# Optimization experiments

Hardware: AMD Instinct MI355X
Metric: run time of the kernel (lower is better)

Reference implementation:

```python
import jax, jax.numpy as jnp
import numpy as np

N = 50000      # nodes
R = 3          # relation types
E = 200000     # edges per relation
DIN, DHID, DOUT = 128, 128, 64


def _hetero_graphconv(x, src, dst, W, b):
    """Sum over relations of dgl GraphConv(norm='both') applied per relation.
    x:[N,d_in], src/dst:[R,E], W:[R,d_in,d_out], b:[R,d_out] -> [N,d_out]"""
    Rr, Ee = src.shape
    n = x.shape[0]
    off = (jnp.arange(Rr) * n)[:, None]            # per-relation segment offset
    src_f = (src + off).reshape(-1)                # [R*E]
    dst_f = (dst + off).reshape(-1)
    ones = jnp.ones((Rr * Ee,), x.dtype)
    out_deg = jax.ops.segment_sum(ones, src_f, num_segments=Rr * n).reshape(Rr, n)
    in_deg = jax.ops.segment_sum(ones, dst_f, num_segments=Rr * n).reshape(Rr, n)
    out_norm = jnp.maximum(out_deg, 1.0) ** -0.5   # dgl clamps deg to min 1
    in_norm = jnp.maximum(in_deg, 1.0) ** -0.5
    # gather src features, scaled by per-relation out-degree norm: [R,E,d_in]
    msgs = x[src] * jnp.take_along_axis(out_norm, src, axis=1)[..., None]
    agg = jax.ops.segment_sum(msgs.reshape(Rr * Ee, -1), dst_f,
                              num_segments=Rr * n).reshape(Rr, n, -1)
    agg = agg * in_norm[..., None]                 # [R,N,d_in]
    # per-relation linear then sum over relations (HeteroGraphConv 'sum')
    return jnp.einsum('rnd,rdo->no', agg, W) + b.sum(axis=0)


def setup_inputs() -> dict:
    key = jax.random.key(0)
    ks = jax.random.split(key, 7)
    x = jax.random.normal(ks[0], (N, DIN), jnp.float32)
    src = jax.random.randint(ks[1], (R, E), 0, N)
    dst = jax.random.randint(ks[2], (R, E), 0, N)
    W1 = jax.random.normal(ks[3], (R, DIN, DHID), jnp.float32) / np.sqrt(DIN).astype(np.float32)
    b1 = jax.random.normal(ks[4], (R, DHID), jnp.float32) * 0.01
    W2 = jax.random.normal(ks[5], (R, DHID, DOUT), jnp.float32) / np.sqrt(DHID).astype(np.float32)
    b2 = jax.random.normal(ks[6], (R, DOUT), jnp.float32) * 0.01
    return {"x": x, "W1": W1, "b1": b1, "W2": W2, "b2": b2, "src": src, "dst": dst}


def reference(x, W1, b1, W2, b2, src, dst):
    h = jax.nn.relu(_hetero_graphconv(x, src, dst, W1, b1))
    return _hetero_graphconv(h, src, dst, W2, b2)
```

## Files before the change

kernel.cpp:

```cpp
#include <hip/hip_runtime.h>

#define N_NODES 50000
#define N_REL   3
#define N_EDGE  200000
#define RN      (N_REL * N_NODES)
#define RE      (N_REL * N_EDGE)

typedef short bf16x8 __attribute__((ext_vector_type(8)));
typedef float f32x4  __attribute__((ext_vector_type(4)));

__global__ __launch_bounds__(256) void deg_count_kernel(
    const int* __restrict__ src, const int* __restrict__ dst,
    float* __restrict__ odeg, float* __restrict__ ideg)
{
    int i = blockIdx.x * 256 + threadIdx.x;
    if (i >= RE) return;
    int r = i / N_EDGE;
    unsafeAtomicAdd(&odeg[r * N_NODES + src[i]], 1.0f);
    unsafeAtomicAdd(&ideg[r * N_NODES + dst[i]], 1.0f);
}

__global__ __launch_bounds__(256) void norm_kernel(
    float* __restrict__ odeg, float* __restrict__ ideg)
{
    int i = blockIdx.x * 256 + threadIdx.x;
    if (i >= RN) return;
    odeg[i] = rsqrtf(fmaxf(odeg[i], 1.0f));
    ideg[i] = rsqrtf(fmaxf(ideg[i], 1.0f));
}

__global__ __launch_bounds__(256) void scan1_kernel(
    const float* __restrict__ ideg, int* __restrict__ off, int* __restrict__ bsums)
{
    __shared__ int tsum[256];
    int tid  = threadIdx.x;
    int base = blockIdx.x * 1024 + tid * 4;
    int c[4], s = 0;
    #pragma unroll
    for (int j = 0; j < 4; ++j) {
        int idx = base + j;
        c[j] = (idx < N_NODES)
             ? (int)(ideg[idx] + ideg[N_NODES + idx] + ideg[2 * N_NODES + idx]) : 0;
        s += c[j];
    }
    tsum[tid] = s;
    __syncthreads();
    #pragma unroll
    for (int d = 1; d < 256; d <<= 1) {
        int v   = tsum[tid];
        int add = (tid >= d) ? tsum[tid - d] : 0;
        __syncthreads();
        tsum[tid] = v + add;
        __syncthreads();
    }
    int run = tsum[tid] - s;
    #pragma unroll
    for (int j = 0; j < 4; ++j) {
        if (base + j < N_NODES) off[base + j] = run;
        run += c[j];
    }
    if (tid == 255) bsums[blockIdx.x] = tsum[255];
}

__global__ __launch_bounds__(256) void scan2_kernel(int* __restrict__ bsums, int nb)
{
    __shared__ int t[256];
    int tid = threadIdx.x;
    int v0  = (tid < nb) ? bsums[tid] : 0;
    t[tid] = v0;
    __syncthreads();
    #pragma unroll
    for (int d = 1; d < 256; d <<= 1) {
        int v   = t[tid];
        int add = (tid >= d) ? t[tid - d] : 0;
        __syncthreads();
        t[tid] = v + add;
        __syncthreads();
    }
    if (tid < nb) bsums[tid] = t[tid] - v0;
}

__global__ __launch_bounds__(256) void scan3_kernel(
    int* __restrict__ off, int* __restrict__ cursor, const int* __restrict__ bsums)
{
    int tid  = threadIdx.x;
    int base = blockIdx.x * 1024 + tid * 4;
    int add  = bsums[blockIdx.x];
    #pragma unroll
    for (int j = 0; j < 4; ++j) {
        if (base + j < N_NODES) {
            int v = off[base + j] + add;
            off[base + j]    = v;
            cursor[base + j] = v;
        }
    }
    if (blockIdx.x == 0 && tid == 0) off[N_NODES] = RE;
}

__global__ __launch_bounds__(256) void fill_kernel(
    const int* __restrict__ src, const int* __restrict__ dst,
    const float* __restrict__ onorm, const float* __restrict__ inorm,
    int* __restrict__ cursor, int2* __restrict__ csr)
{
    int i = blockIdx.x * 256 + threadIdx.x;
    if (i >= N_EDGE) return;
    int r = blockIdx.y;
    int s = src[r * N_EDGE + i];
    int t = dst[r * N_EDGE + i];
    float wv = onorm[r * N_NODES + s] * inorm[r * N_NODES + t];
    int pos = atomicAdd(&cursor[t], 1);
    csr[pos] = make_int2(r * N_NODES + s, __float_as_int(wv));
}

__device__ __forceinline__ unsigned short f2bf(float f) {
    unsigned u = __float_as_uint(f);
    u = (u + 0x7fffu + ((u >> 16) & 1u)) >> 16;
    return (unsigned short)u;
}
__device__ __forceinline__ unsigned pack_bf2(float lo, float hi) {
    return (unsigned)f2bf(lo) | ((unsigned)f2bf(hi) << 16);
}

__global__ __launch_bounds__(256) void wtrans_kernel(
    const float* __restrict__ W, unsigned short* __restrict__ Wtf,
    int ncols, int total)
{
    int i = blockIdx.x * 256 + threadIdx.x;
    if (i >= total) return;
    int rel = i / (128 * ncols);
    int rem = i - rel * 128 * ncols;
    int k   = rem / ncols;
    int n   = rem - k * ncols;
    int f   = (rel * (ncols / 16) + (n >> 4)) * 4 + (k >> 5);
    int idx = f * 512 + ((k & 31) >> 3) * 128 + (n & 15) * 8 + (k & 7);
    Wtf[idx] = f2bf(W[i]);
}

template <bool ABF16, int NCOLS>
__global__ __launch_bounds__(256) void gemm_mfma(
    const void* __restrict__ Av, const unsigned short* __restrict__ Wtf,
    unsigned short* __restrict__ Y, int nrows)
{
    __shared__ unsigned As[64 * 68];
    __shared__ unsigned Ws[2][4096];

    const int tid = threadIdx.x;
    const int mt  = blockIdx.x * 64;
    const uint4* Wt4 = (const uint4*)Wtf;

    if constexpr (ABF16) {
        const uint4* Ab = (const uint4*)Av;
        #pragma unroll
        for (int p = 0; p < 4; ++p) {
            int q   = p * 256 + tid;
            int row = q >> 4, w4 = q & 15;
            int gr  = mt + row;
            uint4 v = make_uint4(0u, 0u, 0u, 0u);
            if (gr < nrows) v = Ab[(size_t)gr * 16 + w4];
            As[row * 68 + w4 * 4 + 0] = v.x;
            As[row * 68 + w4 * 4 + 1] = v.y;
            As[row * 68 + w4 * 4 + 2] = v.z;
            As[row * 68 + w4 * 4 + 3] = v.w;
        }
    } else {
        const float* A = (const float*)Av;
        #pragma unroll
        for (int p = 0; p < 16; ++p) {
            int q   = tid + p * 256;
            int row = q >> 6, wc = q & 63;
            int gr  = mt + row;
            float2 v = make_float2(0.f, 0.f);
            if (gr < nrows) v = *reinterpret_cast<const float2*>(&A[(size_t)gr * 128 + wc * 2]);
            As[row * 68 + wc] = pack_bf2(v.x, v.y);
        }
    }

    #pragma unroll
    for (int p = 0; p < 4; ++p) {
        uint4 v = Wt4[tid + p * 256];
        *reinterpret_cast<uint4*>(&Ws[0][(tid + p * 256) * 4]) = v;
    }
    __syncthreads();

    const int w  = tid >> 6;
    const int l  = tid & 63;
    const int g  = l >> 4;
    const int lr = l & 15;
    const int ar = w * 16 + lr;

    bf16x8 a[4];
    #pragma unroll
    for (int kb = 0; kb < 4; ++kb)
        a[kb] = *reinterpret_cast<const bf16x8*>(&As[ar * 68 + kb * 16 + g * 4]);

    constexpr int TPR  = NCOLS / 16;
    constexpr int NGRP = 3 * NCOLS / 64;
    const int boff = (g * 16 + lr) * 4;

    int cur = 0;
    #pragma unroll 1
    for (int grp = 0; grp < NGRP; ++grp) {
        uint4 st[4];
        if (grp + 1 < NGRP) {
            #pragma unroll
            for (int p = 0; p < 4; ++p)
                st[p] = Wt4[(grp + 1) * 1024 + tid + p * 256];
        }

        f32x4 acc[4];
        #pragma unroll
        for (int ct4 = 0; ct4 < 4; ++ct4) {
            acc[ct4] = (f32x4){0.f, 0.f, 0.f, 0.f};
            #pragma unroll
            for (int kb = 0; kb < 4; ++kb) {
                bf16x8 b = *reinterpret_cast<const bf16x8*>(
                    &Ws[cur][(ct4 * 4 + kb) * 256 + boff]);
                acc[ct4] = __builtin_amdgcn_mfma_f32_16x16x32_bf16(a[kb], b, acc[ct4], 0, 0, 0);
            }
        }

        int gct0 = grp * 4;
        int rel  = gct0 / TPR;
        int cb   = (gct0 % TPR) * 16;
        #pragma unroll
        for (int i = 0; i < 4; ++i) {
            int grow = mt + w * 16 + g * 4 + i;
            if (grow < nrows) {
                size_t rowbase = ((size_t)rel * N_NODES + grow) * NCOLS + cb;
                #pragma unroll
                for (int ct4 = 0; ct4 < 4; ++ct4)
                    Y[rowbase + ct4 * 16 + lr] = f2bf(acc[ct4][i]);
            }
        }

        if (grp + 1 < NGRP) {
            #pragma unroll
            for (int p = 0; p < 4; ++p)
                *reinterpret_cast<uint4*>(&Ws[cur ^ 1][(tid + p * 256) * 4]) = st[p];
        }
        __syncthreads();
        cur ^= 1;
    }
}

__global__ __launch_bounds__(256) void agg128_kernel(
    const unsigned* __restrict__ Y, const int2* __restrict__ csr,
    const int* __restrict__ off, const float* __restrict__ b, unsigned* __restrict__ hbf)
{
    int wid  = (blockIdx.x * 256 + threadIdx.x) >> 6;
    int lane = threadIdx.x & 63;
    if (wid >= N_NODES) return;

    int e = off[wid], end = off[wid + 1];
    float a0 = 0.f, a1 = 0.f;

    for (; e + 8 <= end; e += 8) {
        int2 p[8]; unsigned y[8];
        #pragma unroll
        for (int j = 0; j < 8; ++j) p[j] = csr[e + j];
        #pragma unroll
        for (int j = 0; j < 8; ++j) y[j] = Y[(size_t)p[j].x * 64 + lane];
        #pragma unroll
        for (int j = 0; j < 8; ++j) {
            float wv = __int_as_float(p[j].y);
            a0 = fmaf(wv, __uint_as_float(y[j] << 16), a0);
            a1 = fmaf(wv, __uint_as_float(y[j] & 0xffff0000u), a1);
        }
    }
    if (e + 4 <= end) {
        int2 p[4]; unsigned y[4];
        #pragma unroll
        for (int j = 0; j < 4; ++j) p[j] = csr[e + j];
        #pragma unroll
        for (int j = 0; j < 4; ++j) y[j] = Y[(size_t)p[j].x * 64 + lane];
        #pragma unroll
        for (int j = 0; j < 4; ++j) {
            float wv = __int_as_float(p[j].y);
            a0 = fmaf(wv, __uint_as_float(y[j] << 16), a0);
            a1 = fmaf(wv, __uint_as_float(y[j] & 0xffff0000u), a1);
        }
        e += 4;
    }
    for (; e < end; ++e) {
        int2 p = csr[e];
        float wv = __int_as_float(p.y);
        unsigned y = Y[(size_t)p.x * 64 + lane];
        a0 = fmaf(wv, __uint_as_float(y << 16), a0);
        a1 = fmaf(wv, __uint_as_float(y & 0xffff0000u), a1);
    }

    int d = lane * 2;
    float o0 = a0 + b[d]     + b[128 + d]     + b[256 + d];
    float o1 = a1 + b[d + 1] + b[128 + d + 1] + b[256 + d + 1];
    hbf[(size_t)wid * 64 + lane] = pack_bf2(fmaxf(o0, 0.f), fmaxf(o1, 0.f));
}

__global__ __launch_bounds__(256) void agg64_kernel(
    const unsigned short* __restrict__ Y, const int2* __restrict__ csr,
    const int* __restrict__ off, const float* __restrict__ b, float* __restrict__ out)
{
    int wid  = (blockIdx.x * 256 + threadIdx.x) >> 6;
    int lane = threadIdx.x & 63;
    if (wid >= N_NODES) return;

    int e = off[wid], end = off[wid + 1];
    float a = 0.f;

    for (; e + 8 <= end; e += 8) {
        int2 p[8]; unsigned short y[8];
        #pragma unroll
        for (int j = 0; j < 8; ++j) p[j] = csr[e + j];
        #pragma unroll
        for (int j = 0; j < 8; ++j) y[j] = Y[(size_t)p[j].x * 64 + lane];
        #pragma unroll
        for (int j = 0; j < 8; ++j)
            a = fmaf(__int_as_float(p[j].y),
                     __uint_as_float(((unsigned)y[j]) << 16), a);
    }
    if (e + 4 <= end) {
        int2 p[4]; unsigned short y[4];
        #pragma unroll
        for (int j = 0; j < 4; ++j) p[j] = csr[e + j];
        #pragma unroll
        for (int j = 0; j < 4; ++j) y[j] = Y[(size_t)p[j].x * 64 + lane];
        #pragma unroll
        for (int j = 0; j < 4; ++j)
            a = fmaf(__int_as_float(p[j].y),
                     __uint_as_float(((unsigned)y[j]) << 16), a);
        e += 4;
    }
    for (; e < end; ++e) {
        int2 p = csr[e];
        a = fmaf(__int_as_float(p.y),
                 __uint_as_float(((unsigned)Y[(size_t)p.x * 64 + lane]) << 16), a);
    }

    float bs = b[lane] + b[64 + lane] + b[128 + lane];
    out[(size_t)wid * 64 + lane] = a + bs;
}

extern "C" void kernel_launch(void* const* d_in, const int* in_sizes, int n_in,
                              void* d_out, int out_size, void* d_ws, size_t ws_size,
                              hipStream_t stream)
{
    const float* x   = (const float*)d_in[0];
    const float* W1  = (const float*)d_in[1];
    const float* b1  = (const float*)d_in[2];
    const float* W2  = (const float*)d_in[3];
    const float* b2  = (const float*)d_in[4];
    const int*   src = (const int*)d_in[5];
    const int*   dst = (const int*)d_in[6];
    float*       out = (float*)d_out;

    char* w = (char*)d_ws;
    float* onorm  = (float*)w;                 w += (size_t)RN * 4;
    float* inorm  = (float*)w;                 w += (size_t)RN * 4;
    int*   off    = (int*)w;                   w += (size_t)(N_NODES + 1) * 4;
    int*   cursor = (int*)w;                   w += (size_t)N_NODES * 4;
    int*   bsums  = (int*)w;                   w += 1024;
    w = (char*)(((uintptr_t)w + 255) & ~(uintptr_t)255);
    int2*  csr    = (int2*)w;                  w += (size_t)RE * 8;
    unsigned* hbf = (unsigned*)w;              w += (size_t)N_NODES * 64 * 4;
    unsigned short* Ybf = (unsigned short*)w;  w += (size_t)N_REL * N_NODES * 128 * 2;
    unsigned short* Wt1 = (unsigned short*)w;  w += (size_t)N_REL * 128 * 128 * 2;
    unsigned short* Wt2 = (unsigned short*)w;

    const int SCAN_BLOCKS = (N_NODES + 1023) / 1024;
    const int mtiles = (N_NODES + 63) / 64;

    wtrans_kernel<<<(3 * 128 * 128 + 255) / 256, 256, 0, stream>>>(W1, Wt1, 128, 3 * 128 * 128);
    wtrans_kernel<<<(3 * 128 * 64 + 255) / 256, 256, 0, stream>>>(W2, Wt2, 64, 3 * 128 * 64);

    hipMemsetAsync(onorm, 0, (size_t)2 * RN * 4, stream);
    deg_count_kernel<<<(RE + 255) / 256, 256, 0, stream>>>(src, dst, onorm, inorm);

    scan1_kernel<<<SCAN_BLOCKS, 256, 0, stream>>>(inorm, off, bsums);
    scan2_kernel<<<1, 256, 0, stream>>>(bsums, SCAN_BLOCKS);
    scan3_kernel<<<SCAN_BLOCKS, 256, 0, stream>>>(off, cursor, bsums);

    norm_kernel<<<(RN + 255) / 256, 256, 0, stream>>>(onorm, inorm);
    fill_kernel<<<dim3((N_EDGE + 255) / 256, N_REL), 256, 0, stream>>>(
        src, dst, onorm, inorm, cursor, csr);

    gemm_mfma<false, 128><<<mtiles, 256, 0, stream>>>(x, Wt1, Ybf, N_NODES);
    agg128_kernel<<<(N_NODES + 3) / 4, 256, 0, stream>>>((const unsigned*)Ybf, csr, off, b1, hbf);

    gemm_mfma<true, 64><<<mtiles, 256, 0, stream>>>(hbf, Wt2, Ybf, N_NODES);
    agg64_kernel<<<(N_NODES + 3) / 4, 256, 0, stream>>>(Ybf, csr, off, b2, out);
}
```

Measured before the change: 306.7 us.

## Fuse layer-1 GEMM with degree counting and fold norm into scan

```diff
diff --git a/kernel.cpp b/kernel.cpp
--- a/kernel.cpp
+++ b/kernel.cpp
@@ -5,112 +5,12 @@
 #define N_EDGE  200000
 #define RN      (N_REL * N_NODES)
 #define RE      (N_REL * N_EDGE)
+#define GEMM1_BLKS 782
+#define DEG_BLKS   2344
+#define SCAN_BLOCKS 49
 
 typedef short bf16x8 __attribute__((ext_vector_type(8)));
 typedef float f32x4  __attribute__((ext_vector_type(4)));
-
-__global__ __launch_bounds__(256) void deg_count_kernel(
-    const int* __restrict__ src, const int* __restrict__ dst,
-    float* __restrict__ odeg, float* __restrict__ ideg)
-{
-    int i = blockIdx.x * 256 + threadIdx.x;
-    if (i >= RE) return;
-    int r = i / N_EDGE;
-    unsafeAtomicAdd(&odeg[r * N_NODES + src[i]], 1.0f);
-    unsafeAtomicAdd(&ideg[r * N_NODES + dst[i]], 1.0f);
-}
-
-__global__ __launch_bounds__(256) void norm_kernel(
-    float* __restrict__ odeg, float* __restrict__ ideg)
-{
-    int i = blockIdx.x * 256 + threadIdx.x;
-    if (i >= RN) return;
-    odeg[i] = rsqrtf(fmaxf(odeg[i], 1.0f));
-    ideg[i] = rsqrtf(fmaxf(ideg[i], 1.0f));
-}
-
-__global__ __launch_bounds__(256) void scan1_kernel(
-    const float* __restrict__ ideg, int* __restrict__ off, int* __restrict__ bsums)
-{
-    __shared__ int tsum[256];
-    int tid  = threadIdx.x;
-    int base = blockIdx.x * 1024 + tid * 4;
-    int c[4], s = 0;
-    #pragma unroll
-    for (int j = 0; j < 4; ++j) {
-        int idx = base + j;
-        c[j] = (idx < N_NODES)
-             ? (int)(ideg[idx] + ideg[N_NODES + idx] + ideg[2 * N_NODES + idx]) : 0;
-        s += c[j];
-    }
-    tsum[tid] = s;
-    __syncthreads();
-    #pragma unroll
-    for (int d = 1; d < 256; d <<= 1) {
-        int v   = tsum[tid];
-        int add = (tid >= d) ? tsum[tid - d] : 0;
-        __syncthreads();
-        tsum[tid] = v + add;
-        __syncthreads();
-    }
-    int run = tsum[tid] - s;
-    #pragma unroll
-    for (int j = 0; j < 4; ++j) {
-        if (base + j < N_NODES) off[base + j] = run;
-        run += c[j];
-    }
-    if (tid == 255) bsums[blockIdx.x] = tsum[255];
-}
-
-__global__ __launch_bounds__(256) void scan2_kernel(int* __restrict__ bsums, int nb)
-{
-    __shared__ int t[256];
-    int tid = threadIdx.x;
-    int v0  = (tid < nb) ? bsums[tid] : 0;
-    t[tid] = v0;
-    __syncthreads();
-    #pragma unroll
-    for (int d = 1; d < 256; d <<= 1) {
-        int v   = t[tid];
-        int add = (tid >= d) ? t[tid - d] : 0;
-        __syncthreads();
-        t[tid] = v + add;
-        __syncthreads();
-    }
-    if (tid < nb) bsums[tid] = t[tid] - v0;
-}
-
-__global__ __launch_bounds__(256) void scan3_kernel(
-    int* __restrict__ off, int* __restrict__ cursor, const int* __restrict__ bsums)
-{
-    int tid  = threadIdx.x;
-    int base = blockIdx.x * 1024 + tid * 4;
-    int add  = bsums[blockIdx.x];
-    #pragma unroll
-    for (int j = 0; j < 4; ++j) {
-        if (base + j < N_NODES) {
-            int v = off[base + j] + add;
-            off[base + j]    = v;
-            cursor[base + j] = v;
-        }
-    }
-    if (blockIdx.x == 0 && tid == 0) off[N_NODES] = RE;
-}
-
-__global__ __launch_bounds__(256) void fill_kernel(
-    const int* __restrict__ src, const int* __restrict__ dst,
-    const float* __restrict__ onorm, const float* __restrict__ inorm,
-    int* __restrict__ cursor, int2* __restrict__ csr)
-{
-    int i = blockIdx.x * 256 + threadIdx.x;
-    if (i >= N_EDGE) return;
-    int r = blockIdx.y;
-    int s = src[r * N_EDGE + i];
-    int t = dst[r * N_EDGE + i];
-    float wv = onorm[r * N_NODES + s] * inorm[r * N_NODES + t];
-    int pos = atomicAdd(&cursor[t], 1);
-    csr[pos] = make_int2(r * N_NODES + s, __float_as_int(wv));
-}
 
 __device__ __forceinline__ unsigned short f2bf(float f) {
     unsigned u = __float_as_uint(f);
@@ -121,12 +21,9 @@
     return (unsigned)f2bf(lo) | ((unsigned)f2bf(hi) << 16);
 }
 
-__global__ __launch_bounds__(256) void wtrans_kernel(
-    const float* __restrict__ W, unsigned short* __restrict__ Wtf,
-    int ncols, int total)
-{
-    int i = blockIdx.x * 256 + threadIdx.x;
-    if (i >= total) return;
+__device__ __forceinline__ void wtrans_one(
+    const float* __restrict__ W, unsigned short* __restrict__ Wtf, int ncols, int i)
+{
     int rel = i / (128 * ncols);
     int rem = i - rel * 128 * ncols;
     int k   = rem / ncols;
@@ -136,16 +33,26 @@
     Wtf[idx] = f2bf(W[i]);
 }
 
+__global__ __launch_bounds__(256) void wtrans2_kernel(
+    const float* __restrict__ W1, unsigned short* __restrict__ Wt1,
+    const float* __restrict__ W2, unsigned short* __restrict__ Wt2)
+{
+    int i = blockIdx.x * 256 + threadIdx.x;
+    if (i < 3 * 128 * 128) {
+        wtrans_one(W1, Wt1, 128, i);
+    } else {
+        int j = i - 3 * 128 * 128;
+        if (j < 3 * 128 * 64) wtrans_one(W2, Wt2, 64, j);
+    }
+}
+
 template <bool ABF16, int NCOLS>
-__global__ __launch_bounds__(256) void gemm_mfma(
+__device__ __forceinline__ void gemm_body(
     const void* __restrict__ Av, const unsigned short* __restrict__ Wtf,
-    unsigned short* __restrict__ Y, int nrows)
-{
-    __shared__ unsigned As[64 * 68];
-    __shared__ unsigned Ws[2][4096];
-
+    unsigned short* __restrict__ Y, int nrows, int mt,
+    unsigned* As, unsigned* Ws0, unsigned* Ws1)
+{
     const int tid = threadIdx.x;
-    const int mt  = blockIdx.x * 64;
     const uint4* Wt4 = (const uint4*)Wtf;
 
     if constexpr (ABF16) {
@@ -178,7 +85,7 @@
     #pragma unroll
     for (int p = 0; p < 4; ++p) {
         uint4 v = Wt4[tid + p * 256];
-        *reinterpret_cast<uint4*>(&Ws[0][(tid + p * 256) * 4]) = v;
+        *reinterpret_cast<uint4*>(&Ws0[(tid + p * 256) * 4]) = v;
     }
     __syncthreads();
 
@@ -197,7 +104,8 @@
     constexpr int NGRP = 3 * NCOLS / 64;
     const int boff = (g * 16 + lr) * 4;
 
-    int cur = 0;
+    unsigned* wc_buf = Ws0;
+    unsigned* wn_buf = Ws1;
     #pragma unroll 1
     for (int grp = 0; grp < NGRP; ++grp) {
         uint4 st[4];
@@ -214,7 +122,7 @@
             #pragma unroll
             for (int kb = 0; kb < 4; ++kb) {
                 bf16x8 b = *reinterpret_cast<const bf16x8*>(
-                    &Ws[cur][(ct4 * 4 + kb) * 256 + boff]);
+                    &wc_buf[(ct4 * 4 + kb) * 256 + boff]);
                 acc[ct4] = __builtin_amdgcn_mfma_f32_16x16x32_bf16(a[kb], b, acc[ct4], 0, 0, 0);
             }
         }
@@ -236,11 +144,132 @@
         if (grp + 1 < NGRP) {
             #pragma unroll
             for (int p = 0; p < 4; ++p)
-                *reinterpret_cast<uint4*>(&Ws[cur ^ 1][(tid + p * 256) * 4]) = st[p];
+                *reinterpret_cast<uint4*>(&wn_buf[(tid + p * 256) * 4]) = st[p];
         }
         __syncthreads();
-        cur ^= 1;
-    }
+        unsigned* t = wc_buf; wc_buf = wn_buf; wn_buf = t;
+    }
+}
+
+__global__ __launch_bounds__(256) void fused_gemm1_deg(
+    const float* __restrict__ x, const unsigned short* __restrict__ Wt1,
+    unsigned short* __restrict__ Y,
+    const int* __restrict__ src, const int* __restrict__ dst,
+    float* __restrict__ odeg, float* __restrict__ ideg)
+{
+    __shared__ unsigned As[64 * 68];
+    __shared__ unsigned Ws[2][4096];
+
+    if (blockIdx.x < GEMM1_BLKS) {
+        gemm_body<false, 128>(x, Wt1, Y, N_NODES, blockIdx.x * 64, As, Ws[0], Ws[1]);
+    } else {
+        int i = (blockIdx.x - GEMM1_BLKS) * 256 + threadIdx.x;
+        if (i < RE) {
+            int r = i / N_EDGE;
+            unsafeAtomicAdd(&odeg[r * N_NODES + src[i]], 1.0f);
+            unsafeAtomicAdd(&ideg[r * N_NODES + dst[i]], 1.0f);
+        }
+    }
+}
+
+template <bool ABF16, int NCOLS>
+__global__ __launch_bounds__(256) void gemm_mfma(
+    const void* __restrict__ Av, const unsigned short* __restrict__ Wtf,
+    unsigned short* __restrict__ Y, int nrows)
+{
+    __shared__ unsigned As[64 * 68];
+    __shared__ unsigned Ws[2][4096];
+    gemm_body<ABF16, NCOLS>(Av, Wtf, Y, nrows, blockIdx.x * 64, As, Ws[0], Ws[1]);
+}
+
+__global__ __launch_bounds__(256) void scan1_kernel(
+    const float* __restrict__ ideg, int* __restrict__ off, int* __restrict__ bsums)
+{
+    __shared__ int tsum[256];
+    int tid  = threadIdx.x;
+    int base = blockIdx.x * 1024 + tid * 4;
+    int c[4], s = 0;
+    #pragma unroll
+    for (int j = 0; j < 4; ++j) {
+        int idx = base + j;
+        c[j] = (idx < N_NODES)
+             ? (int)(ideg[idx] + ideg[N_NODES + idx] + ideg[2 * N_NODES + idx]) : 0;
+        s += c[j];
+    }
+    tsum[tid] = s;
+    __syncthreads();
+    #pragma unroll
+    for (int d = 1; d < 256; d <<= 1) {
+        int v   = tsum[tid];
+        int add = (tid >= d) ? tsum[tid - d] : 0;
+        __syncthreads();
+        tsum[tid] = v + add;
+        __syncthreads();
+    }
+    int run = tsum[tid] - s;
+    #pragma unroll
+    for (int j = 0; j < 4; ++j) {
+        if (base + j < N_NODES) off[base + j] = run;
+        run += c[j];
+    }
+    if (tid == 255) bsums[blockIdx.x] = tsum[255];
+}
+
+__global__ __launch_bounds__(256) void scan2_kernel(int* __restrict__ bsums, int nb)
+{
+    __shared__ int t[256];
+    int tid = threadIdx.x;
+    int v0  = (tid < nb) ? bsums[tid] : 0;
+    t[tid] = v0;
+    __syncthreads();
+    #pragma unroll
+    for (int d = 1; d < 256; d <<= 1) {
+        int v   = t[tid];
+        int add = (tid >= d) ? t[tid - d] : 0;
+        __syncthreads();
+        t[tid] = v + add;
+        __syncthreads();
+    }
+    if (tid < nb) bsums[tid] = t[tid] - v0;
+}
+
+__global__ __launch_bounds__(256) void scan3_kernel(
+    int* __restrict__ off, int* __restrict__ cursor, const int* __restrict__ bsums,
+    float* __restrict__ odeg, float* __restrict__ ideg)
+{
+    int tid  = threadIdx.x;
+    int base = blockIdx.x * 1024 + tid * 4;
+    int add  = bsums[blockIdx.x];
+    #pragma unroll
+    for (int j = 0; j < 4; ++j) {
+        if (base + j < N_NODES) {
+            int v = off[base + j] + add;
+            off[base + j]    = v;
+            cursor[base + j] = v;
+        }
+    }
+    if (blockIdx.x == 0 && tid == 0) off[N_NODES] = RE;
+
+    int t = blockIdx.x * 256 + tid;
+    for (int q = t; q < RN; q += SCAN_BLOCKS * 256) {
+        odeg[q] = rsqrtf(fmaxf(odeg[q], 1.0f));
+        ideg[q] = rsqrtf(fmaxf(ideg[q], 1.0f));
+    }
+}
+
+__global__ __launch_bounds__(256) void fill_kernel(
+    const int* __restrict__ src, const int* __restrict__ dst,
+    const float* __restrict__ onorm, const float* __restrict__ inorm,
+    int* __restrict__ cursor, int2* __restrict__ csr)
+{
+    int i = blockIdx.x * 256 + threadIdx.x;
+    if (i >= N_EDGE) return;
+    int r = blockIdx.y;
+    int s = src[r * N_EDGE + i];
+    int t = dst[r * N_EDGE + i];
+    float wv = onorm[r * N_NODES + s] * inorm[r * N_NODES + t];
+    int pos = atomicAdd(&cursor[t], 1);
+    csr[pos] = make_int2(r * N_NODES + s, __float_as_int(wv));
 }
 
 __global__ __launch_bounds__(256) void agg128_kernel(
@@ -365,26 +394,22 @@
     unsigned short* Wt1 = (unsigned short*)w;  w += (size_t)N_REL * 128 * 128 * 2;
     unsigned short* Wt2 = (unsigned short*)w;
 
-    const int SCAN_BLOCKS = (N_NODES + 1023) / 1024;
-    const int mtiles = (N_NODES + 63) / 64;
-
-    wtrans_kernel<<<(3 * 128 * 128 + 255) / 256, 256, 0, stream>>>(W1, Wt1, 128, 3 * 128 * 128);
-    wtrans_kernel<<<(3 * 128 * 64 + 255) / 256, 256, 0, stream>>>(W2, Wt2, 64, 3 * 128 * 64);
+    wtrans2_kernel<<<(3 * 128 * 128 + 3 * 128 * 64 + 255) / 256, 256, 0, stream>>>(
+        W1, Wt1, W2, Wt2);
 
     hipMemsetAsync(onorm, 0, (size_t)2 * RN * 4, stream);
-    deg_count_kernel<<<(RE + 255) / 256, 256, 0, stream>>>(src, dst, onorm, inorm);
+    fused_gemm1_deg<<<GEMM1_BLKS + DEG_BLKS, 256, 0, stream>>>(
+        x, Wt1, Ybf, src, dst, onorm, inorm);
 
     scan1_kernel<<<SCAN_BLOCKS, 256, 0, stream>>>(inorm, off, bsums);
     scan2_kernel<<<1, 256, 0, stream>>>(bsums, SCAN_BLOCKS);
-    scan3_kernel<<<SCAN_BLOCKS, 256, 0, stream>>>(off, cursor, bsums);
-
-    norm_kernel<<<(RN + 255) / 256, 256, 0, stream>>>(onorm, inorm);
+    scan3_kernel<<<SCAN_BLOCKS, 256, 0, stream>>>(off, cursor, bsums, onorm, inorm);
+
     fill_kernel<<<dim3((N_EDGE + 255) / 256, N_REL), 256, 0, stream>>>(
         src, dst, onorm, inorm, cursor, csr);
 
-    gemm_mfma<false, 128><<<mtiles, 256, 0, stream>>>(x, Wt1, Ybf, N_NODES);
     agg128_kernel<<<(N_NODES + 3) / 4, 256, 0, stream>>>((const unsigned*)Ybf, csr, off, b1, hbf);
 
-    gemm_mfma<true, 64><<<mtiles, 256, 0, stream>>>(hbf, Wt2, Ybf, N_NODES);
+    gemm_mfma<true, 64><<<GEMM1_BLKS, 256, 0, stream>>>(hbf, Wt2, Ybf, N_NODES);
     agg64_kernel<<<(N_NODES + 3) / 4, 256, 0, stream>>>(Ybf, csr, off, b2, out);
 }
```

Result: faster. 290.8 us (-5.2%).
